# Performance work log

Measured on AMD Instinct MI355X. Metric: run time of the kernel, lower is better.

## Reference

```python
import jax, jax.numpy as jnp
import numpy as np

H = 2048
E = 64
TOP_K = 4
EPS = 1e-6


def _rms_norm(x, eps):
    # Gemma RMSNorm without scale: compute in fp32, cast back.
    x32 = x.astype(jnp.float32)
    var = jnp.mean(x32 * x32, axis=-1, keepdims=True)
    return (x32 * jax.lax.rsqrt(var + eps)).astype(x.dtype)


def setup_inputs() -> dict:
    key = jax.random.key(0)
    k1, k2 = jax.random.split(key)
    hidden_states = jax.random.normal(k1, (4, 4096, H), dtype=jnp.float32)
    proj_w = jax.random.normal(k2, (E, H), dtype=jnp.float32) * (H ** -0.5)
    scale = jnp.ones((H,), dtype=jnp.float32)
    per_expert_scale = jnp.ones((E,), dtype=jnp.float32)
    return {"hidden_states": hidden_states, "proj_w": proj_w,
            "scale": scale, "per_expert_scale": per_expert_scale}


def reference(hidden_states, proj_w, scale, per_expert_scale):
    scalar_root_size = H ** (-0.5)
    h = _rms_norm(hidden_states, EPS) * scale * scalar_root_size  # [B,S,H]
    expert_scores = jnp.einsum('bsh,eh->bse', h, proj_w)          # [B,S,E]
    router_probabilities = jax.nn.softmax(expert_scores, axis=-1)
    top_k_weights, top_k_index = jax.lax.top_k(router_probabilities, TOP_K)
    top_k_weights = top_k_weights / jnp.sum(top_k_weights, axis=-1, keepdims=True)
    top_k_weights = top_k_weights * per_expert_scale[top_k_index]
    return router_probabilities, top_k_weights, top_k_index
```

## Files before the change

### kernel.cpp

```cpp
#include <hip/hip_runtime.h>
#include <cstddef>

#define HDIM 2048
#define NE 64
#define TOPK 4

typedef short bf16x8 __attribute__((ext_vector_type(8)));
typedef float f32x4 __attribute__((ext_vector_type(4)));

__device__ __forceinline__ void split3(float a, unsigned short& h0,
                                       unsigned short& h1, unsigned short& h2) {
    unsigned int u = __float_as_uint(a);
    h0 = (unsigned short)(u >> 16);
    float f0 = __uint_as_float(u & 0xffff0000u);
    float r1 = a - f0;
    unsigned int v = __float_as_uint(r1);
    h1 = (unsigned short)(v >> 16);
    float f1 = __uint_as_float(v & 0xffff0000u);
    float r2 = r1 - f1;
    h2 = (unsigned short)(__float_as_uint(r2) >> 16);
}

__global__ __launch_bounds__(256) void prep_b_kernel(
    const float* __restrict__ w, const float* __restrict__ scale,
    unsigned short* __restrict__ wtb)
{
    const int s = blockIdx.x;
    const int n = threadIdx.x >> 6;
    const int l = threadIdx.x & 63;
    const int e = 16 * n + (l & 15);
    const int k = 32 * s + 8 * (l >> 4);
    unsigned short h0[8], h1[8], h2[8];
    #pragma unroll
    for (int j = 0; j < 8; ++j) {
        float v = w[(size_t)e * HDIM + k + j] * scale[k + j];
        split3(v, h0[j], h1[j], h2[j]);
    }
    size_t off = ((size_t)s * 4 + n) * 512 + (size_t)l * 8;
    #pragma unroll
    for (int j = 0; j < 8; ++j) {
        wtb[off + j]          = h0[j];
        wtb[131072 + off + j] = h1[j];
        wtb[262144 + off + j] = h2[j];
    }
}

__global__ __launch_bounds__(256, 2) void fused_router_kernel(
    const float* __restrict__ x, const unsigned short* __restrict__ wtb,
    const float* __restrict__ pes,
    float* __restrict__ probs, float* __restrict__ tkw, float* __restrict__ tki)
{
    __shared__ float Sp[4][32 * 65];
    __shared__ float SQp[4][32];
    __shared__ float Sl[32 * 65];
    __shared__ float Pl[32 * 65];
    __shared__ float FN[32];
    __shared__ float RS[32];

    const int tid = threadIdx.x;
    const int kh = tid >> 6;
    const int l = tid & 63;
    const int tok0 = blockIdx.x * 32;
    const int m = l & 15;
    const int g = l >> 4;

    const float* xr0 = x + (size_t)(tok0 + m) * HDIM + 512 * kh + 8 * g;
    const float* xr1 = xr0 + (size_t)16 * HDIM;
    const unsigned short* wb = wtb + (size_t)(16 * kh) * 2048 + (size_t)l * 8;

    f32x4 acc0[4], acc1[4];
    #pragma unroll
    for (int n = 0; n < 4; ++n) {
        acc0[n] = (f32x4){0.f, 0.f, 0.f, 0.f};
        acc1[n] = (f32x4){0.f, 0.f, 0.f, 0.f};
    }
    float ssq0 = 0.f, ssq1 = 0.f;

    float4 Aq[2][4];
    bf16x8 Bb[2][12];

#define LOADA(buf, s) { \
        Aq[buf][0] = *(const float4*)(xr0 + 32 * (s)); \
        Aq[buf][1] = *(const float4*)(xr0 + 32 * (s) + 4); \
        Aq[buf][2] = *(const float4*)(xr1 + 32 * (s)); \
        Aq[buf][3] = *(const float4*)(xr1 + 32 * (s) + 4); }
#define LOADB(buf, s) { \
        const unsigned short* bs_ = wb + (size_t)(s) * 2048; \
        _Pragma("unroll") \
        for (int n = 0; n < 4; ++n) { \
            Bb[buf][3*n + 0] = *(const bf16x8*)(bs_ + n * 512); \
            Bb[buf][3*n + 1] = *(const bf16x8*)(bs_ + n * 512 + 131072); \
            Bb[buf][3*n + 2] = *(const bf16x8*)(bs_ + n * 512 + 262144); } }

    LOADA(0, 0);
    LOADB(0, 0);

    #pragma unroll
    for (int s = 0; s < 16; ++s) {
        const int cur = s & 1, nxt = cur ^ 1;
        if (s + 1 < 16) { LOADA(nxt, s + 1); LOADB(nxt, s + 1); }

        float af0[8], af1[8];
        *(float4*)af0 = Aq[cur][0]; *(float4*)(af0 + 4) = Aq[cur][1];
        *(float4*)af1 = Aq[cur][2]; *(float4*)(af1 + 4) = Aq[cur][3];
        unsigned short p0[8], p1[8], p2[8], q0[8], q1[8], q2[8];
        #pragma unroll
        for (int j = 0; j < 8; ++j) {
            split3(af0[j], p0[j], p1[j], p2[j]);
            split3(af1[j], q0[j], q1[j], q2[j]);
            ssq0 = fmaf(af0[j], af0[j], ssq0);
            ssq1 = fmaf(af1[j], af1[j], ssq1);
        }
        bf16x8 a0, a1, a2, c0, c1, c2;
        #pragma unroll
        for (int j = 0; j < 8; ++j) {
            a0[j] = (short)p0[j]; a1[j] = (short)p1[j]; a2[j] = (short)p2[j];
            c0[j] = (short)q0[j]; c1[j] = (short)q1[j]; c2[j] = (short)q2[j];
        }
        #pragma unroll
        for (int n = 0; n < 4; ++n) {
            bf16x8 b0 = Bb[cur][3*n + 0];
            bf16x8 b1 = Bb[cur][3*n + 1];
            bf16x8 b2 = Bb[cur][3*n + 2];
            acc0[n] = __builtin_amdgcn_mfma_f32_16x16x32_bf16(a0, b0, acc0[n], 0, 0, 0);
            acc0[n] = __builtin_amdgcn_mfma_f32_16x16x32_bf16(a0, b1, acc0[n], 0, 0, 0);
            acc0[n] = __builtin_amdgcn_mfma_f32_16x16x32_bf16(a1, b0, acc0[n], 0, 0, 0);
            acc0[n] = __builtin_amdgcn_mfma_f32_16x16x32_bf16(a1, b1, acc0[n], 0, 0, 0);
            acc0[n] = __builtin_amdgcn_mfma_f32_16x16x32_bf16(a0, b2, acc0[n], 0, 0, 0);
            acc0[n] = __builtin_amdgcn_mfma_f32_16x16x32_bf16(a2, b0, acc0[n], 0, 0, 0);
            acc1[n] = __builtin_amdgcn_mfma_f32_16x16x32_bf16(c0, b0, acc1[n], 0, 0, 0);
            acc1[n] = __builtin_amdgcn_mfma_f32_16x16x32_bf16(c0, b1, acc1[n], 0, 0, 0);
            acc1[n] = __builtin_amdgcn_mfma_f32_16x16x32_bf16(c1, b0, acc1[n], 0, 0, 0);
            acc1[n] = __builtin_amdgcn_mfma_f32_16x16x32_bf16(c1, b1, acc1[n], 0, 0, 0);
            acc1[n] = __builtin_amdgcn_mfma_f32_16x16x32_bf16(c0, b2, acc1[n], 0, 0, 0);
            acc1[n] = __builtin_amdgcn_mfma_f32_16x16x32_bf16(c2, b0, acc1[n], 0, 0, 0);
        }
    }
#undef LOADA
#undef LOADB

    ssq0 += __shfl_xor(ssq0, 16, 64);
    ssq0 += __shfl_xor(ssq0, 32, 64);
    ssq1 += __shfl_xor(ssq1, 16, 64);
    ssq1 += __shfl_xor(ssq1, 32, 64);

    #pragma unroll
    for (int n = 0; n < 4; ++n)
        #pragma unroll
        for (int r = 0; r < 4; ++r) {
            Sp[kh][(4 * g + r) * 65 + 16 * n + m]      = acc0[n][r];
            Sp[kh][(16 + 4 * g + r) * 65 + 16 * n + m] = acc1[n][r];
        }
    if (l < 16) {
        SQp[kh][m]      = ssq0;
        SQp[kh][16 + m] = ssq1;
    }
    __syncthreads();

    if (tid < 32) {
        float st = (SQp[0][tid] + SQp[1][tid]) + (SQp[2][tid] + SQp[3][tid]);
        FN[tid] = rsqrtf(st * (1.0f / HDIM) + 1e-6f) * 0.022097086912079612f;
    }
    __syncthreads();

    #pragma unroll
    for (int qq = 0; qq < 2; qq++) {
        int f = tid + 256 * qq;
        int mr = f >> 4;
        int e4 = (f & 15) * 4;
        float4 t0 = *(const float4*)&Sp[0][mr * 65 + e4];
        float4 t1 = *(const float4*)&Sp[1][mr * 65 + e4];
        float4 t2 = *(const float4*)&Sp[2][mr * 65 + e4];
        float4 t3 = *(const float4*)&Sp[3][mr * 65 + e4];
        float fn = FN[mr];
        Sl[mr * 65 + e4 + 0] = ((t0.x + t1.x) + (t2.x + t3.x)) * fn;
        Sl[mr * 65 + e4 + 1] = ((t0.y + t1.y) + (t2.y + t3.y)) * fn;
        Sl[mr * 65 + e4 + 2] = ((t0.z + t1.z) + (t2.z + t3.z)) * fn;
        Sl[mr * 65 + e4 + 3] = ((t0.w + t1.w) + (t2.w + t3.w)) * fn;
    }
    __syncthreads();

    if (tid < 32) {
        const int mm = tid;
        float mx = -3.0e38f;
        for (int e = 0; e < NE; e++) mx = fmaxf(mx, Sl[mm * 65 + e]);
        float sum = 0.f;
        for (int e = 0; e < NE; e++) {
            float p = __expf(Sl[mm * 65 + e] - mx);
            Pl[mm * 65 + e] = p;
            sum += p;
        }
        RS[mm] = 1.0f / sum;
    }
    __syncthreads();

    #pragma unroll
    for (int qq = 0; qq < 2; qq++) {
        int f = tid + 256 * qq;
        int mr = f >> 4;
        int e0 = (f & 15) * 4;
        float rs = RS[mr];
        float4 pv;
        pv.x = Pl[mr * 65 + e0 + 0] * rs;
        pv.y = Pl[mr * 65 + e0 + 1] * rs;
        pv.z = Pl[mr * 65 + e0 + 2] * rs;
        pv.w = Pl[mr * 65 + e0 + 3] * rs;
        *(float4*)&probs[(size_t)(tok0 + mr) * NE + e0] = pv;
    }

    if (tid < 32) {
        const int mm = tid;
        float wvv[TOPK]; int idx[TOPK];
        float wsum = 0.f;
        #pragma unroll
        for (int kk = 0; kk < TOPK; ++kk) {
            float best = -3.0e38f; int bi = 0;
            for (int e = 0; e < NE; e++) {
                float v = Sl[mm * 65 + e];
                if (v > best) { best = v; bi = e; }
            }
            Sl[mm * 65 + bi] = -3.4e38f;
            float p = Pl[mm * 65 + bi];
            wvv[kk] = p; idx[kk] = bi; wsum += p;
        }
        float inv = 1.0f / wsum;
        size_t ob = (size_t)(tok0 + mm) * TOPK;
        #pragma unroll
        for (int kk = 0; kk < TOPK; kk++) {
            tkw[ob + kk] = wvv[kk] * inv * pes[idx[kk]];
            tki[ob + kk] = (float)idx[kk];
        }
    }
}

extern "C" void kernel_launch(void* const* d_in, const int* in_sizes, int n_in,
                              void* d_out, int out_size, void* d_ws, size_t ws_size,
                              hipStream_t stream) {
    const float* x     = (const float*)d_in[0];
    const float* w     = (const float*)d_in[1];
    const float* scale = (const float*)d_in[2];
    const float* pes   = (const float*)d_in[3];
    const int tokens = in_sizes[0] / HDIM;

    float* probs = (float*)d_out;
    float* tkw   = probs + (size_t)tokens * NE;
    float* tki   = tkw + (size_t)tokens * TOPK;

    unsigned short* wtb = (unsigned short*)d_ws;

    prep_b_kernel<<<HDIM / 32, 256, 0, stream>>>(w, scale, wtb);

    const int grid = tokens / 32;
    fused_router_kernel<<<grid, 256, 0, stream>>>(x, wtb, pes, probs, tkw, tki);
}
```

Before: 47.53 us.

## Process 64 tokens per 512-thread block with 8-way K split

Doubles the token tile per block to 64 rows and the K split to 8 waves of 256 columns each, so every loaded weight fragment feeds four 16-row MFMA tiles instead of two. This halves global and cache traffic for the split weights per token. The final logits are reduced in place into the first partial buffer, dropping a separate shared array. The trade-offs are more accumulator registers per thread, larger shared memory (about 150KB), one block per CU, and half as many blocks (256), which can leave CUs idle and limit latency hiding.

```diff
diff --git a/kernel.cpp b/kernel.cpp
--- a/kernel.cpp
+++ b/kernel.cpp
@@ -45,45 +45,41 @@
     }
 }
 
-__global__ __launch_bounds__(256, 2) void fused_router_kernel(
+__global__ __launch_bounds__(512, 1) void fused_router_kernel(
     const float* __restrict__ x, const unsigned short* __restrict__ wtb,
     const float* __restrict__ pes,
     float* __restrict__ probs, float* __restrict__ tkw, float* __restrict__ tki)
 {
-    __shared__ float Sp[4][32 * 65];
-    __shared__ float SQp[4][32];
-    __shared__ float Sl[32 * 65];
-    __shared__ float Pl[32 * 65];
-    __shared__ float FN[32];
-    __shared__ float RS[32];
+    __shared__ float Sp[8][64 * 65];
+    __shared__ float Pl[64 * 65];
+    __shared__ float SQp[8][64];
+    __shared__ float FN[64];
+    __shared__ float RS[64];
 
     const int tid = threadIdx.x;
     const int kh = tid >> 6;
     const int l = tid & 63;
-    const int tok0 = blockIdx.x * 32;
+    const int tok0 = blockIdx.x * 64;
     const int m = l & 15;
     const int g = l >> 4;
 
-    const float* xr0 = x + (size_t)(tok0 + m) * HDIM + 512 * kh + 8 * g;
-    const float* xr1 = xr0 + (size_t)16 * HDIM;
-    const unsigned short* wb = wtb + (size_t)(16 * kh) * 2048 + (size_t)l * 8;
-
-    f32x4 acc0[4], acc1[4];
-    #pragma unroll
-    for (int n = 0; n < 4; ++n) {
-        acc0[n] = (f32x4){0.f, 0.f, 0.f, 0.f};
-        acc1[n] = (f32x4){0.f, 0.f, 0.f, 0.f};
-    }
-    float ssq0 = 0.f, ssq1 = 0.f;
-
-    float4 Aq[2][4];
+    const float* xr0 = x + (size_t)(tok0 + m) * HDIM + 256 * kh + 8 * g;
+    const unsigned short* wb = wtb + (size_t)(8 * kh) * 2048 + (size_t)l * 8;
+
+    f32x4 acc[4][4];
+    #pragma unroll
+    for (int t = 0; t < 4; ++t)
+        #pragma unroll
+        for (int n = 0; n < 4; ++n) acc[t][n] = (f32x4){0.f, 0.f, 0.f, 0.f};
+    float ssq[4] = {0.f, 0.f, 0.f, 0.f};
+
+    float4 Aq[2][8];
     bf16x8 Bb[2][12];
 
-#define LOADA(buf, s) { \
-        Aq[buf][0] = *(const float4*)(xr0 + 32 * (s)); \
-        Aq[buf][1] = *(const float4*)(xr0 + 32 * (s) + 4); \
-        Aq[buf][2] = *(const float4*)(xr1 + 32 * (s)); \
-        Aq[buf][3] = *(const float4*)(xr1 + 32 * (s) + 4); }
+#define LOADA(buf, s) { _Pragma("unroll") \
+        for (int t = 0; t < 4; ++t) { \
+            Aq[buf][2*t]     = *(const float4*)(xr0 + (size_t)(16*t) * HDIM + 32 * (s)); \
+            Aq[buf][2*t + 1] = *(const float4*)(xr0 + (size_t)(16*t) * HDIM + 32 * (s) + 4); } }
 #define LOADB(buf, s) { \
         const unsigned short* bs_ = wb + (size_t)(s) * 2048; \
         _Pragma("unroll") \
@@ -96,91 +92,95 @@
     LOADB(0, 0);
 
     #pragma unroll
-    for (int s = 0; s < 16; ++s) {
+    for (int s = 0; s < 8; ++s) {
         const int cur = s & 1, nxt = cur ^ 1;
-        if (s + 1 < 16) { LOADA(nxt, s + 1); LOADB(nxt, s + 1); }
-
-        float af0[8], af1[8];
-        *(float4*)af0 = Aq[cur][0]; *(float4*)(af0 + 4) = Aq[cur][1];
-        *(float4*)af1 = Aq[cur][2]; *(float4*)(af1 + 4) = Aq[cur][3];
-        unsigned short p0[8], p1[8], p2[8], q0[8], q1[8], q2[8];
-        #pragma unroll
-        for (int j = 0; j < 8; ++j) {
-            split3(af0[j], p0[j], p1[j], p2[j]);
-            split3(af1[j], q0[j], q1[j], q2[j]);
-            ssq0 = fmaf(af0[j], af0[j], ssq0);
-            ssq1 = fmaf(af1[j], af1[j], ssq1);
-        }
-        bf16x8 a0, a1, a2, c0, c1, c2;
-        #pragma unroll
-        for (int j = 0; j < 8; ++j) {
-            a0[j] = (short)p0[j]; a1[j] = (short)p1[j]; a2[j] = (short)p2[j];
-            c0[j] = (short)q0[j]; c1[j] = (short)q1[j]; c2[j] = (short)q2[j];
-        }
-        #pragma unroll
-        for (int n = 0; n < 4; ++n) {
-            bf16x8 b0 = Bb[cur][3*n + 0];
-            bf16x8 b1 = Bb[cur][3*n + 1];
-            bf16x8 b2 = Bb[cur][3*n + 2];
-            acc0[n] = __builtin_amdgcn_mfma_f32_16x16x32_bf16(a0, b0, acc0[n], 0, 0, 0);
-            acc0[n] = __builtin_amdgcn_mfma_f32_16x16x32_bf16(a0, b1, acc0[n], 0, 0, 0);
-            acc0[n] = __builtin_amdgcn_mfma_f32_16x16x32_bf16(a1, b0, acc0[n], 0, 0, 0);
-            acc0[n] = __builtin_amdgcn_mfma_f32_16x16x32_bf16(a1, b1, acc0[n], 0, 0, 0);
-            acc0[n] = __builtin_amdgcn_mfma_f32_16x16x32_bf16(a0, b2, acc0[n], 0, 0, 0);
-            acc0[n] = __builtin_amdgcn_mfma_f32_16x16x32_bf16(a2, b0, acc0[n], 0, 0, 0);
-            acc1[n] = __builtin_amdgcn_mfma_f32_16x16x32_bf16(c0, b0, acc1[n], 0, 0, 0);
-            acc1[n] = __builtin_amdgcn_mfma_f32_16x16x32_bf16(c0, b1, acc1[n], 0, 0, 0);
-            acc1[n] = __builtin_amdgcn_mfma_f32_16x16x32_bf16(c1, b0, acc1[n], 0, 0, 0);
-            acc1[n] = __builtin_amdgcn_mfma_f32_16x16x32_bf16(c1, b1, acc1[n], 0, 0, 0);
-            acc1[n] = __builtin_amdgcn_mfma_f32_16x16x32_bf16(c0, b2, acc1[n], 0, 0, 0);
-            acc1[n] = __builtin_amdgcn_mfma_f32_16x16x32_bf16(c2, b0, acc1[n], 0, 0, 0);
+        if (s + 1 < 8) { LOADB(nxt, s + 1); LOADA(nxt, s + 1); }
+
+        #pragma unroll
+        for (int t = 0; t < 4; ++t) {
+            float af[8];
+            *(float4*)af = Aq[cur][2*t]; *(float4*)(af + 4) = Aq[cur][2*t + 1];
+            unsigned short p0[8], p1[8], p2[8];
+            #pragma unroll
+            for (int j = 0; j < 8; ++j) {
+                split3(af[j], p0[j], p1[j], p2[j]);
+                ssq[t] = fmaf(af[j], af[j], ssq[t]);
+            }
+            bf16x8 a0, a1, a2;
+            #pragma unroll
+            for (int j = 0; j < 8; ++j) {
+                a0[j] = (short)p0[j]; a1[j] = (short)p1[j]; a2[j] = (short)p2[j];
+            }
+            #pragma unroll
+            for (int n = 0; n < 4; ++n) {
+                bf16x8 b0 = Bb[cur][3*n + 0];
+                bf16x8 b1 = Bb[cur][3*n + 1];
+                bf16x8 b2 = Bb[cur][3*n + 2];
+                acc[t][n] = __builtin_amdgcn_mfma_f32_16x16x32_bf16(a0, b0, acc[t][n], 0, 0, 0);
+                acc[t][n] = __builtin_amdgcn_mfma_f32_16x16x32_bf16(a0, b1, acc[t][n], 0, 0, 0);
+                acc[t][n] = __builtin_amdgcn_mfma_f32_16x16x32_bf16(a1, b0, acc[t][n], 0, 0, 0);
+                acc[t][n] = __builtin_amdgcn_mfma_f32_16x16x32_bf16(a1, b1, acc[t][n], 0, 0, 0);
+                acc[t][n] = __builtin_amdgcn_mfma_f32_16x16x32_bf16(a0, b2, acc[t][n], 0, 0, 0);
+                acc[t][n] = __builtin_amdgcn_mfma_f32_16x16x32_bf16(a2, b0, acc[t][n], 0, 0, 0);
+            }
         }
     }
 #undef LOADA
 #undef LOADB
 
-    ssq0 += __shfl_xor(ssq0, 16, 64);
-    ssq0 += __shfl_xor(ssq0, 32, 64);
-    ssq1 += __shfl_xor(ssq1, 16, 64);
-    ssq1 += __shfl_xor(ssq1, 32, 64);
-
-    #pragma unroll
-    for (int n = 0; n < 4; ++n)
-        #pragma unroll
-        for (int r = 0; r < 4; ++r) {
-            Sp[kh][(4 * g + r) * 65 + 16 * n + m]      = acc0[n][r];
-            Sp[kh][(16 + 4 * g + r) * 65 + 16 * n + m] = acc1[n][r];
-        }
+    #pragma unroll
+    for (int t = 0; t < 4; ++t) {
+        ssq[t] += __shfl_xor(ssq[t], 16, 64);
+        ssq[t] += __shfl_xor(ssq[t], 32, 64);
+    }
+
+    #pragma unroll
+    for (int t = 0; t < 4; ++t)
+        #pragma unroll
+        for (int n = 0; n < 4; ++n)
+            #pragma unroll
+            for (int r = 0; r < 4; ++r)
+                Sp[kh][(16*t + 4*g + r) * 65 + 16*n + m] = acc[t][n][r];
     if (l < 16) {
-        SQp[kh][m]      = ssq0;
-        SQp[kh][16 + m] = ssq1;
-    }
-    __syncthreads();
-
-    if (tid < 32) {
-        float st = (SQp[0][tid] + SQp[1][tid]) + (SQp[2][tid] + SQp[3][tid]);
-        FN[tid] = rsqrtf(st * (1.0f / HDIM) + 1e-6f) * 0.022097086912079612f;
+        #pragma unroll
+        for (int t = 0; t < 4; ++t) SQp[kh][16*t + m] = ssq[t];
+    }
+    __syncthreads();
+
+    if (tid < 64) {
+        float q0 = (SQp[0][tid] + SQp[1][tid]) + (SQp[2][tid] + SQp[3][tid]);
+        float q1 = (SQp[4][tid] + SQp[5][tid]) + (SQp[6][tid] + SQp[7][tid]);
+        FN[tid] = rsqrtf((q0 + q1) * (1.0f / HDIM) + 1e-6f) * 0.022097086912079612f;
     }
     __syncthreads();
 
     #pragma unroll
     for (int qq = 0; qq < 2; qq++) {
-        int f = tid + 256 * qq;
+        int f = tid + 512 * qq;
         int mr = f >> 4;
         int e4 = (f & 15) * 4;
-        float4 t0 = *(const float4*)&Sp[0][mr * 65 + e4];
-        float4 t1 = *(const float4*)&Sp[1][mr * 65 + e4];
-        float4 t2 = *(const float4*)&Sp[2][mr * 65 + e4];
-        float4 t3 = *(const float4*)&Sp[3][mr * 65 + e4];
+        int base = mr * 65 + e4;
+        float4 t0 = *(const float4*)&Sp[0][base];
+        float4 t1 = *(const float4*)&Sp[1][base];
+        float4 t2 = *(const float4*)&Sp[2][base];
+        float4 t3 = *(const float4*)&Sp[3][base];
+        float4 t4 = *(const float4*)&Sp[4][base];
+        float4 t5 = *(const float4*)&Sp[5][base];
+        float4 t6 = *(const float4*)&Sp[6][base];
+        float4 t7 = *(const float4*)&Sp[7][base];
         float fn = FN[mr];
-        Sl[mr * 65 + e4 + 0] = ((t0.x + t1.x) + (t2.x + t3.x)) * fn;
-        Sl[mr * 65 + e4 + 1] = ((t0.y + t1.y) + (t2.y + t3.y)) * fn;
-        Sl[mr * 65 + e4 + 2] = ((t0.z + t1.z) + (t2.z + t3.z)) * fn;
-        Sl[mr * 65 + e4 + 3] = ((t0.w + t1.w) + (t2.w + t3.w)) * fn;
-    }
-    __syncthreads();
-
-    if (tid < 32) {
+        float4 sv;
+        sv.x = (((t0.x + t1.x) + (t2.x + t3.x)) + ((t4.x + t5.x) + (t6.x + t7.x))) * fn;
+        sv.y = (((t0.y + t1.y) + (t2.y + t3.y)) + ((t4.y + t5.y) + (t6.y + t7.y))) * fn;
+        sv.z = (((t0.z + t1.z) + (t2.z + t3.z)) + ((t4.z + t5.z) + (t6.z + t7.z))) * fn;
+        sv.w = (((t0.w + t1.w) + (t2.w + t3.w)) + ((t4.w + t5.w) + (t6.w + t7.w))) * fn;
+        *(float4*)&Sp[0][base] = sv;
+    }
+    __syncthreads();
+
+    float* Sl = &Sp[0][0];
+
+    if (tid < 64) {
         const int mm = tid;
         float mx = -3.0e38f;
         for (int e = 0; e < NE; e++) mx = fmaxf(mx, Sl[mm * 65 + e]);
@@ -196,7 +196,7 @@
 
     #pragma unroll
     for (int qq = 0; qq < 2; qq++) {
-        int f = tid + 256 * qq;
+        int f = tid + 512 * qq;
         int mr = f >> 4;
         int e0 = (f & 15) * 4;
         float rs = RS[mr];
@@ -208,7 +208,7 @@
         *(float4*)&probs[(size_t)(tok0 + mr) * NE + e0] = pv;
     }
 
-    if (tid < 32) {
+    if (tid < 64) {
         const int mm = tid;
         float wvv[TOPK]; int idx[TOPK];
         float wsum = 0.f;
@@ -250,6 +250,6 @@
 
     prep_b_kernel<<<HDIM / 32, 256, 0, stream>>>(w, scale, wtb);
 
-    const int grid = tokens / 32;
-    fused_router_kernel<<<grid, 256, 0, stream>>>(x, wtb, pes, probs, tkw, tki);
-}
+    const int grid = tokens / 64;
+    fused_router_kernel<<<grid, 512, 0, stream>>>(x, wtb, pes, probs, tkw, tki);
+}
```

Measured after the change: 44.97 us. 5.4% less time.

## Split K across eight waves per block and drop B register double-buffering

Applied to the files above, without the earlier changes.

The fused router kernel now launches 512 threads per block, so eight waves split the 2048-wide reduction into 256-wide chunks with 8 steps each instead of four waves doing 16 steps. The weight fragments are no longer double-buffered in registers; they are loaded at the start of each step, which frees VGPRs for the larger block. The partial-sum LDS buffer grows to eight slices, and the first slice is reused as the logits buffer in place of a separate array. The intent is more waves in flight to hide memory latency, at the cost of more LDS per block, a larger cross-wave reduction, and exposed B-load latency inside each step.

```diff
diff --git a/kernel.cpp b/kernel.cpp
--- a/kernel.cpp
+++ b/kernel.cpp
@@ -45,15 +45,14 @@
     }
 }
 
-__global__ __launch_bounds__(256, 2) void fused_router_kernel(
+__global__ __launch_bounds__(512, 2) void fused_router_kernel(
     const float* __restrict__ x, const unsigned short* __restrict__ wtb,
     const float* __restrict__ pes,
     float* __restrict__ probs, float* __restrict__ tkw, float* __restrict__ tki)
 {
-    __shared__ float Sp[4][32 * 65];
-    __shared__ float SQp[4][32];
-    __shared__ float Sl[32 * 65];
+    __shared__ float Sp[8][32 * 65];
     __shared__ float Pl[32 * 65];
+    __shared__ float SQp[8][32];
     __shared__ float FN[32];
     __shared__ float RS[32];
 
@@ -64,9 +63,9 @@
     const int m = l & 15;
     const int g = l >> 4;
 
-    const float* xr0 = x + (size_t)(tok0 + m) * HDIM + 512 * kh + 8 * g;
+    const float* xr0 = x + (size_t)(tok0 + m) * HDIM + 256 * kh + 8 * g;
     const float* xr1 = xr0 + (size_t)16 * HDIM;
-    const unsigned short* wb = wtb + (size_t)(16 * kh) * 2048 + (size_t)l * 8;
+    const unsigned short* wb = wtb + (size_t)(8 * kh) * 2048 + (size_t)l * 8;
 
     f32x4 acc0[4], acc1[4];
     #pragma unroll
@@ -77,28 +76,28 @@
     float ssq0 = 0.f, ssq1 = 0.f;
 
     float4 Aq[2][4];
-    bf16x8 Bb[2][12];
+    bf16x8 Bb[12];
 
 #define LOADA(buf, s) { \
         Aq[buf][0] = *(const float4*)(xr0 + 32 * (s)); \
         Aq[buf][1] = *(const float4*)(xr0 + 32 * (s) + 4); \
         Aq[buf][2] = *(const float4*)(xr1 + 32 * (s)); \
         Aq[buf][3] = *(const float4*)(xr1 + 32 * (s) + 4); }
-#define LOADB(buf, s) { \
+#define LOADB(s) { \
         const unsigned short* bs_ = wb + (size_t)(s) * 2048; \
         _Pragma("unroll") \
         for (int n = 0; n < 4; ++n) { \
-            Bb[buf][3*n + 0] = *(const bf16x8*)(bs_ + n * 512); \
-            Bb[buf][3*n + 1] = *(const bf16x8*)(bs_ + n * 512 + 131072); \
-            Bb[buf][3*n + 2] = *(const bf16x8*)(bs_ + n * 512 + 262144); } }
+            Bb[3*n + 0] = *(const bf16x8*)(bs_ + n * 512); \
+            Bb[3*n + 1] = *(const bf16x8*)(bs_ + n * 512 + 131072); \
+            Bb[3*n + 2] = *(const bf16x8*)(bs_ + n * 512 + 262144); } }
 
     LOADA(0, 0);
-    LOADB(0, 0);
-
-    #pragma unroll
-    for (int s = 0; s < 16; ++s) {
+
+    #pragma unroll
+    for (int s = 0; s < 8; ++s) {
         const int cur = s & 1, nxt = cur ^ 1;
-        if (s + 1 < 16) { LOADA(nxt, s + 1); LOADB(nxt, s + 1); }
+        LOADB(s);
+        if (s + 1 < 8) LOADA(nxt, s + 1);
 
         float af0[8], af1[8];
         *(float4*)af0 = Aq[cur][0]; *(float4*)(af0 + 4) = Aq[cur][1];
@@ -119,9 +118,9 @@
         }
         #pragma unroll
         for (int n = 0; n < 4; ++n) {
-            bf16x8 b0 = Bb[cur][3*n + 0];
-            bf16x8 b1 = Bb[cur][3*n + 1];
-            bf16x8 b2 = Bb[cur][3*n + 2];
+            bf16x8 b0 = Bb[3*n + 0];
+            bf16x8 b1 = Bb[3*n + 1];
+            bf16x8 b2 = Bb[3*n + 2];
             acc0[n] = __builtin_amdgcn_mfma_f32_16x16x32_bf16(a0, b0, acc0[n], 0, 0, 0);
             acc0[n] = __builtin_amdgcn_mfma_f32_16x16x32_bf16(a0, b1, acc0[n], 0, 0, 0);
             acc0[n] = __builtin_amdgcn_mfma_f32_16x16x32_bf16(a1, b0, acc0[n], 0, 0, 0);
@@ -158,27 +157,36 @@
     __syncthreads();
 
     if (tid < 32) {
-        float st = (SQp[0][tid] + SQp[1][tid]) + (SQp[2][tid] + SQp[3][tid]);
-        FN[tid] = rsqrtf(st * (1.0f / HDIM) + 1e-6f) * 0.022097086912079612f;
-    }
-    __syncthreads();
-
-    #pragma unroll
-    for (int qq = 0; qq < 2; qq++) {
-        int f = tid + 256 * qq;
+        float q0 = (SQp[0][tid] + SQp[1][tid]) + (SQp[2][tid] + SQp[3][tid]);
+        float q1 = (SQp[4][tid] + SQp[5][tid]) + (SQp[6][tid] + SQp[7][tid]);
+        FN[tid] = rsqrtf((q0 + q1) * (1.0f / HDIM) + 1e-6f) * 0.022097086912079612f;
+    }
+    __syncthreads();
+
+    {
+        int f = tid;
         int mr = f >> 4;
         int e4 = (f & 15) * 4;
-        float4 t0 = *(const float4*)&Sp[0][mr * 65 + e4];
-        float4 t1 = *(const float4*)&Sp[1][mr * 65 + e4];
-        float4 t2 = *(const float4*)&Sp[2][mr * 65 + e4];
-        float4 t3 = *(const float4*)&Sp[3][mr * 65 + e4];
+        int base = mr * 65 + e4;
+        float4 t0 = *(const float4*)&Sp[0][base];
+        float4 t1 = *(const float4*)&Sp[1][base];
+        float4 t2 = *(const float4*)&Sp[2][base];
+        float4 t3 = *(const float4*)&Sp[3][base];
+        float4 t4 = *(const float4*)&Sp[4][base];
+        float4 t5 = *(const float4*)&Sp[5][base];
+        float4 t6 = *(const float4*)&Sp[6][base];
+        float4 t7 = *(const float4*)&Sp[7][base];
         float fn = FN[mr];
-        Sl[mr * 65 + e4 + 0] = ((t0.x + t1.x) + (t2.x + t3.x)) * fn;
-        Sl[mr * 65 + e4 + 1] = ((t0.y + t1.y) + (t2.y + t3.y)) * fn;
-        Sl[mr * 65 + e4 + 2] = ((t0.z + t1.z) + (t2.z + t3.z)) * fn;
-        Sl[mr * 65 + e4 + 3] = ((t0.w + t1.w) + (t2.w + t3.w)) * fn;
-    }
-    __syncthreads();
+        float4 sv;
+        sv.x = (((t0.x + t1.x) + (t2.x + t3.x)) + ((t4.x + t5.x) + (t6.x + t7.x))) * fn;
+        sv.y = (((t0.y + t1.y) + (t2.y + t3.y)) + ((t4.y + t5.y) + (t6.y + t7.y))) * fn;
+        sv.z = (((t0.z + t1.z) + (t2.z + t3.z)) + ((t4.z + t5.z) + (t6.z + t7.z))) * fn;
+        sv.w = (((t0.w + t1.w) + (t2.w + t3.w)) + ((t4.w + t5.w) + (t6.w + t7.w))) * fn;
+        *(float4*)&Sp[0][base] = sv;
+    }
+    __syncthreads();
+
+    float* Sl = &Sp[0][0];
 
     if (tid < 32) {
         const int mm = tid;
@@ -194,9 +202,8 @@
     }
     __syncthreads();
 
-    #pragma unroll
-    for (int qq = 0; qq < 2; qq++) {
-        int f = tid + 256 * qq;
+    {
+        int f = tid;
         int mr = f >> 4;
         int e0 = (f & 15) * 4;
         float rs = RS[mr];
@@ -251,5 +258,5 @@
     prep_b_kernel<<<HDIM / 32, 256, 0, stream>>>(w, scale, wtb);
 
     const int grid = tokens / 32;
-    fused_router_kernel<<<grid, 256, 0, stream>>>(x, wtb, pes, probs, tkw, tki);
-}
+    fused_router_kernel<<<grid, 512, 0, stream>>>(x, wtb, pes, probs, tkw, tki);
+}
```

Result: slower. 50.44 us (+6.1%).

## Split router GEMM across K into separate kernel with global partials and finish kernel

Applied to the files above, without the earlier changes.

The fused router kernel is split into a GEMM kernel and a finish kernel. When the workspace is large enough, each 32-token tile's K dimension is also split across two blocks. Partial score sums and sum-of-squares go to global memory (the probs output buffer is reused for one partial), and a second kernel reduces them, then runs the normalization, softmax and top-k. The intent is to double the block count for better CU occupancy and to raise wave priority around the MFMA section. The cost is extra global traffic for the partials plus one more kernel launch.

```diff
diff --git a/kernel.cpp b/kernel.cpp
--- a/kernel.cpp
+++ b/kernel.cpp
@@ -4,6 +4,7 @@
 #define HDIM 2048
 #define NE 64
 #define TOPK 4
+#define BM2 32
 
 typedef short bf16x8 __attribute__((ext_vector_type(8)));
 typedef float f32x4 __attribute__((ext_vector_type(4)));
@@ -45,28 +46,28 @@
     }
 }
 
-__global__ __launch_bounds__(256, 2) void fused_router_kernel(
+template<int KSPLIT>
+__global__ __launch_bounds__(256) void gemm21_kernel(
     const float* __restrict__ x, const unsigned short* __restrict__ wtb,
-    const float* __restrict__ pes,
-    float* __restrict__ probs, float* __restrict__ tkw, float* __restrict__ tki)
+    float* __restrict__ sp0,
+    float* __restrict__ spws,
+    float* __restrict__ sq,
+    int tokens)
 {
-    __shared__ float Sp[4][32 * 65];
-    __shared__ float SQp[4][32];
-    __shared__ float Sl[32 * 65];
-    __shared__ float Pl[32 * 65];
-    __shared__ float FN[32];
-    __shared__ float RS[32];
-
+    constexpr int NST = 16 / KSPLIT;
     const int tid = threadIdx.x;
     const int kh = tid >> 6;
     const int l = tid & 63;
-    const int tok0 = blockIdx.x * 32;
+    const int khalf = (KSPLIT == 2) ? (blockIdx.x & 1) : 0;
+    const int tok0 = ((KSPLIT == 2) ? (blockIdx.x >> 1) : blockIdx.x) * 32;
+    const int p = khalf * 4 + kh;
+    const int k0 = p * (NST * 32);
     const int m = l & 15;
     const int g = l >> 4;
 
-    const float* xr0 = x + (size_t)(tok0 + m) * HDIM + 512 * kh + 8 * g;
+    const float* xr0 = x + (size_t)(tok0 + m) * HDIM + k0 + 8 * g;
     const float* xr1 = xr0 + (size_t)16 * HDIM;
-    const unsigned short* wb = wtb + (size_t)(16 * kh) * 2048 + (size_t)l * 8;
+    const unsigned short* wb = wtb + (size_t)(p * NST) * 2048 + (size_t)l * 8;
 
     f32x4 acc0[4], acc1[4];
     #pragma unroll
@@ -96,9 +97,9 @@
     LOADB(0, 0);
 
     #pragma unroll
-    for (int s = 0; s < 16; ++s) {
+    for (int s = 0; s < NST; ++s) {
         const int cur = s & 1, nxt = cur ^ 1;
-        if (s + 1 < 16) { LOADA(nxt, s + 1); LOADB(nxt, s + 1); }
+        if (s + 1 < NST) { LOADA(nxt, s + 1); LOADB(nxt, s + 1); }
 
         float af0[8], af1[8];
         *(float4*)af0 = Aq[cur][0]; *(float4*)(af0 + 4) = Aq[cur][1];
@@ -117,6 +118,7 @@
             a0[j] = (short)p0[j]; a1[j] = (short)p1[j]; a2[j] = (short)p2[j];
             c0[j] = (short)q0[j]; c1[j] = (short)q1[j]; c2[j] = (short)q2[j];
         }
+        __builtin_amdgcn_s_setprio(1);
         #pragma unroll
         for (int n = 0; n < 4; ++n) {
             bf16x8 b0 = Bb[cur][3*n + 0];
@@ -135,6 +137,7 @@
             acc1[n] = __builtin_amdgcn_mfma_f32_16x16x32_bf16(c0, b2, acc1[n], 0, 0, 0);
             acc1[n] = __builtin_amdgcn_mfma_f32_16x16x32_bf16(c2, b0, acc1[n], 0, 0, 0);
         }
+        __builtin_amdgcn_s_setprio(0);
     }
 #undef LOADA
 #undef LOADB
@@ -143,23 +146,45 @@
     ssq0 += __shfl_xor(ssq0, 32, 64);
     ssq1 += __shfl_xor(ssq1, 16, 64);
     ssq1 += __shfl_xor(ssq1, 32, 64);
-
+    if (g == 0) {
+        sq[(size_t)p * tokens + tok0 + m]      = ssq0;
+        sq[(size_t)p * tokens + tok0 + 16 + m] = ssq1;
+    }
+
+    float* sp = (p == 0) ? sp0 : (spws + (size_t)(p - 1) * tokens * NE);
     #pragma unroll
     for (int n = 0; n < 4; ++n)
         #pragma unroll
         for (int r = 0; r < 4; ++r) {
-            Sp[kh][(4 * g + r) * 65 + 16 * n + m]      = acc0[n][r];
-            Sp[kh][(16 + 4 * g + r) * 65 + 16 * n + m] = acc1[n][r];
-        }
-    if (l < 16) {
-        SQp[kh][m]      = ssq0;
-        SQp[kh][16 + m] = ssq1;
-    }
-    __syncthreads();
-
-    if (tid < 32) {
-        float st = (SQp[0][tid] + SQp[1][tid]) + (SQp[2][tid] + SQp[3][tid]);
-        FN[tid] = rsqrtf(st * (1.0f / HDIM) + 1e-6f) * 0.022097086912079612f;
+            sp[(size_t)(tok0 + 4 * g + r) * NE + 16 * n + m]      = acc0[n][r];
+            sp[(size_t)(tok0 + 16 + 4 * g + r) * NE + 16 * n + m] = acc1[n][r];
+        }
+}
+
+template<int KS>
+__global__ __launch_bounds__(256) void finish21_kernel(
+    const float* __restrict__ sp0, const float* __restrict__ spws,
+    const float* __restrict__ sq, const float* __restrict__ pes,
+    float* __restrict__ probs, float* __restrict__ tkw, float* __restrict__ tki,
+    int tokens)
+{
+    __shared__ float Sl[BM2 * 65];
+    __shared__ float Pl[BM2 * 65];
+    __shared__ float FN[BM2];
+    __shared__ float RS[BM2];
+
+    const int tid = threadIdx.x;
+    const int tok0 = blockIdx.x * BM2;
+
+    if (tid < BM2) {
+        float q[KS];
+        #pragma unroll
+        for (int i = 0; i < KS; i++) q[i] = sq[(size_t)i * tokens + tok0 + tid];
+        #pragma unroll
+        for (int st = 1; st < KS; st <<= 1)
+            #pragma unroll
+            for (int i = 0; i < KS; i += 2 * st) q[i] += q[i + st];
+        FN[tid] = rsqrtf(q[0] * (1.0f / HDIM) + 1e-6f) * 0.022097086912079612f;
     }
     __syncthreads();
 
@@ -167,28 +192,36 @@
     for (int qq = 0; qq < 2; qq++) {
         int f = tid + 256 * qq;
         int mr = f >> 4;
-        int e4 = (f & 15) * 4;
-        float4 t0 = *(const float4*)&Sp[0][mr * 65 + e4];
-        float4 t1 = *(const float4*)&Sp[1][mr * 65 + e4];
-        float4 t2 = *(const float4*)&Sp[2][mr * 65 + e4];
-        float4 t3 = *(const float4*)&Sp[3][mr * 65 + e4];
+        int e4 = f & 15;
+        float4 t[KS];
+        t[0] = ((const float4*)sp0)[(size_t)(tok0 + mr) * (NE / 4) + e4];
+        #pragma unroll
+        for (int i = 1; i < KS; i++)
+            t[i] = ((const float4*)(spws + (size_t)(i - 1) * tokens * NE))
+                       [(size_t)(tok0 + mr) * (NE / 4) + e4];
+        #pragma unroll
+        for (int st = 1; st < KS; st <<= 1)
+            #pragma unroll
+            for (int i = 0; i < KS; i += 2 * st) {
+                t[i].x += t[i + st].x; t[i].y += t[i + st].y;
+                t[i].z += t[i + st].z; t[i].w += t[i + st].w;
+            }
         float fn = FN[mr];
-        Sl[mr * 65 + e4 + 0] = ((t0.x + t1.x) + (t2.x + t3.x)) * fn;
-        Sl[mr * 65 + e4 + 1] = ((t0.y + t1.y) + (t2.y + t3.y)) * fn;
-        Sl[mr * 65 + e4 + 2] = ((t0.z + t1.z) + (t2.z + t3.z)) * fn;
-        Sl[mr * 65 + e4 + 3] = ((t0.w + t1.w) + (t2.w + t3.w)) * fn;
+        int base = mr * 65 + e4 * 4;
+        Sl[base + 0] = t[0].x * fn; Sl[base + 1] = t[0].y * fn;
+        Sl[base + 2] = t[0].z * fn; Sl[base + 3] = t[0].w * fn;
     }
     __syncthreads();
 
-    if (tid < 32) {
+    if (tid < BM2) {
         const int mm = tid;
         float mx = -3.0e38f;
         for (int e = 0; e < NE; e++) mx = fmaxf(mx, Sl[mm * 65 + e]);
         float sum = 0.f;
         for (int e = 0; e < NE; e++) {
-            float p = __expf(Sl[mm * 65 + e] - mx);
-            Pl[mm * 65 + e] = p;
-            sum += p;
+            float pp = __expf(Sl[mm * 65 + e] - mx);
+            Pl[mm * 65 + e] = pp;
+            sum += pp;
         }
         RS[mm] = 1.0f / sum;
     }
@@ -208,9 +241,9 @@
         *(float4*)&probs[(size_t)(tok0 + mr) * NE + e0] = pv;
     }
 
-    if (tid < 32) {
+    if (tid < BM2) {
         const int mm = tid;
-        float wvv[TOPK]; int idx[TOPK];
+        float wv[TOPK]; int idx[TOPK];
         float wsum = 0.f;
         #pragma unroll
         for (int kk = 0; kk < TOPK; ++kk) {
@@ -220,14 +253,14 @@
                 if (v > best) { best = v; bi = e; }
             }
             Sl[mm * 65 + bi] = -3.4e38f;
-            float p = Pl[mm * 65 + bi];
-            wvv[kk] = p; idx[kk] = bi; wsum += p;
+            float pp = Pl[mm * 65 + bi];
+            wv[kk] = pp; idx[kk] = bi; wsum += pp;
         }
         float inv = 1.0f / wsum;
         size_t ob = (size_t)(tok0 + mm) * TOPK;
         #pragma unroll
         for (int kk = 0; kk < TOPK; kk++) {
-            tkw[ob + kk] = wvv[kk] * inv * pes[idx[kk]];
+            tkw[ob + kk] = wv[kk] * inv * pes[idx[kk]];
             tki[ob + kk] = (float)idx[kk];
         }
     }
@@ -246,10 +279,29 @@
     float* tkw   = probs + (size_t)tokens * NE;
     float* tki   = tkw + (size_t)tokens * TOPK;
 
+    const size_t wtbF = 196608;
+    const size_t spN  = (size_t)tokens * NE;
     unsigned short* wtb = (unsigned short*)d_ws;
+    auto need = [&](int kp) {
+        return (wtbF + (size_t)(4 * kp - 1) * spN + (size_t)(4 * kp) * tokens) * sizeof(float);
+    };
+    const int KSPLIT = (ws_size >= need(2)) ? 2 : 1;
+
+    float* spws = (float*)d_ws + wtbF;
+    float* sq   = spws + (size_t)(4 * KSPLIT - 1) * spN;
+    float* sp0  = probs;
 
     prep_b_kernel<<<HDIM / 32, 256, 0, stream>>>(w, scale, wtb);
 
-    const int grid = tokens / 32;
-    fused_router_kernel<<<grid, 256, 0, stream>>>(x, wtb, pes, probs, tkw, tki);
-}
+    const int grid1 = (tokens / 32) * KSPLIT;
+    if (KSPLIT == 2)
+        gemm21_kernel<2><<<grid1, 256, 0, stream>>>(x, wtb, sp0, spws, sq, tokens);
+    else
+        gemm21_kernel<1><<<grid1, 256, 0, stream>>>(x, wtb, sp0, spws, sq, tokens);
+
+    const int grid2 = tokens / BM2;
+    if (KSPLIT == 2)
+        finish21_kernel<8><<<grid2, 256, 0, stream>>>(sp0, spws, sq, pes, probs, tkw, tki, tokens);
+    else
+        finish21_kernel<4><<<grid2, 256, 0, stream>>>(sp0, spws, sq, pes, probs, tkw, tki, tokens);
+}
```

New measurement: 57.17 us. 20.3% more time.
